# Optimization experiments

Measured on AMD Instinct MI355X. Metric: run time of the kernel, lower is better.

## Reference

```python
import jax, jax.numpy as jnp
import numpy as np


def setup_inputs() -> dict:
    key = jax.random.key(0)
    k1, k2 = jax.random.split(key)
    B, N, M, D = 4, 8192, 8192, 3
    pred_points = jax.random.normal(k1, (B, N, D), dtype=jnp.float32)
    gt_points = jax.random.normal(k2, (B, M, D), dtype=jnp.float32)
    return {"pred_points": pred_points, "gt_points": gt_points}


def reference(pred_points, gt_points):
    p2 = jnp.sum(pred_points * pred_points, axis=-1)  # [B, N]
    g2 = jnp.sum(gt_points * gt_points, axis=-1)      # [B, M]
    cross = jnp.einsum("bnd,bmd->bnm", pred_points, gt_points)  # [B, N, M]
    d2 = p2[:, :, None] + g2[:, None, :] - 2.0 * cross
    dist = jnp.sqrt(jnp.maximum(d2, 0.0))             # [B, N, M]
    min_pred_to_gt = jnp.min(dist, axis=-1)           # [B, N]
    min_gt_to_pred = jnp.min(dist, axis=-2)           # [B, M]
    return min_pred_to_gt.mean() + min_gt_to_pred.mean()
```

## Files before the change

### kernel.cpp

```cpp
#include <hip/hip_runtime.h>


#define B_ 4
#define N_ 8192
#define QPT 4
#define THREADS 256

__global__ __launch_bounds__(THREADS) void chamfer_min2(
    const float* __restrict__ pred, const float* __restrict__ gt,
    float* __restrict__ partial) {
  extern __shared__ float4 sh[];
  const int S = gridDim.y;
  const int TPB = N_ / S;
  const int dirb = blockIdx.z;
  const int dir = dirb >> 2;
  const int b = dirb & 3;

  const float* qsrc = (dir == 0 ? pred : gt) + (size_t)b * N_ * 3;
  const float* tsrc = (dir == 0 ? gt : pred) + (size_t)b * N_ * 3;

  const float* tb = tsrc + (size_t)blockIdx.y * TPB * 3;
  for (int g = 0; g < TPB; g += THREADS * 4) {
    const int p0 = g + threadIdx.x * 4;
    if (p0 < TPB) {
      const float4 f0 = *(const float4*)(tb + 3 * p0);
      const float4 f1 = *(const float4*)(tb + 3 * p0 + 4);
      const float4 f2 = *(const float4*)(tb + 3 * p0 + 8);
      sh[p0 + 0] = make_float4(f0.x, f0.y, f0.z,
                               fmaf(f0.x, f0.x, fmaf(f0.y, f0.y, f0.z * f0.z)));
      sh[p0 + 1] = make_float4(f0.w, f1.x, f1.y,
                               fmaf(f0.w, f0.w, fmaf(f1.x, f1.x, f1.y * f1.y)));
      sh[p0 + 2] = make_float4(f1.z, f1.w, f2.x,
                               fmaf(f1.z, f1.z, fmaf(f1.w, f1.w, f2.x * f2.x)));
      sh[p0 + 3] = make_float4(f2.y, f2.z, f2.w,
                               fmaf(f2.y, f2.y, fmaf(f2.z, f2.z, f2.w * f2.w)));
    }
  }
  __syncthreads();

  const int qbase = blockIdx.x * (THREADS * QPT) + threadIdx.x;
  float nx[QPT], ny[QPT], nz[QPT], q2[QPT];
#pragma unroll
  for (int k = 0; k < QPT; ++k) {
    const int qi = qbase + k * THREADS;
    const float x = qsrc[3 * qi], y = qsrc[3 * qi + 1], z = qsrc[3 * qi + 2];
    nx[k] = -2.0f * x; ny[k] = -2.0f * y; nz[k] = -2.0f * z;
    q2[k] = fmaf(x, x, fmaf(y, y, z * z));
  }

  float acc0[QPT], acc1[QPT];
#pragma unroll
  for (int k = 0; k < QPT; ++k) { acc0[k] = 3.4e38f; acc1[k] = 3.4e38f; }

  for (int j = 0; j < TPB; j += 4) {
    const float4 t0 = sh[j + 0];
    const float4 t1 = sh[j + 1];
    const float4 t2 = sh[j + 2];
    const float4 t3 = sh[j + 3];
#pragma unroll
    for (int k = 0; k < QPT; ++k) {
      const float s0 = fmaf(nx[k], t0.x, fmaf(ny[k], t0.y, fmaf(nz[k], t0.z, t0.w)));
      const float s1 = fmaf(nx[k], t1.x, fmaf(ny[k], t1.y, fmaf(nz[k], t1.z, t1.w)));
      const float s2 = fmaf(nx[k], t2.x, fmaf(ny[k], t2.y, fmaf(nz[k], t2.z, t2.w)));
      const float s3 = fmaf(nx[k], t3.x, fmaf(ny[k], t3.y, fmaf(nz[k], t3.z, t3.w)));
      acc0[k] = fminf(fminf(acc0[k], s0), s1);
      acc1[k] = fminf(fminf(acc1[k], s2), s3);
    }
  }

  float* dst = partial + ((size_t)dirb * S + blockIdx.y) * N_;
#pragma unroll
  for (int k = 0; k < QPT; ++k) {
    const int qi = qbase + k * THREADS;
    dst[qi] = fmaxf(q2[k] + fminf(acc0[k], acc1[k]), 0.0f);
  }
}

#define FBLOCKS 64
__global__ __launch_bounds__(256) void chamfer_finalize(
    const float* __restrict__ partial, float* __restrict__ out, int S) {
  float sum = 0.0f;
  const int total = 8 * N_;
  for (int f = blockIdx.x * 256 + threadIdx.x; f < total; f += FBLOCKS * 256) {
    const int dirb = f >> 13;
    const int qi = f & (N_ - 1);
    const float* p = partial + (size_t)dirb * S * N_ + qi;
    float v = p[0];
    for (int s = 1; s < S; ++s) v = fminf(v, p[(size_t)s * N_]);
    sum += sqrtf(v);
  }
#pragma unroll
  for (int off = 32; off > 0; off >>= 1) sum += __shfl_down(sum, off, 64);
  __shared__ float ws[4];
  const int lane = threadIdx.x & 63;
  const int wid = threadIdx.x >> 6;
  if (lane == 0) ws[wid] = sum;
  __syncthreads();
  if (threadIdx.x == 0) {
    atomicAdd(out, ((ws[0] + ws[1]) + (ws[2] + ws[3])) * (1.0f / 32768.0f));
  }
}

extern "C" void kernel_launch(void* const* d_in, const int* in_sizes, int n_in,
                              void* d_out, int out_size, void* d_ws, size_t ws_size,
                              hipStream_t stream) {
  const float* pred = (const float*)d_in[0];
  const float* gt   = (const float*)d_in[1];
  float* out = (float*)d_out;
  float* partial = (float*)d_ws;

  int S = 4;
  if (ws_size >= (size_t)8 * 16 * N_ * sizeof(float)) S = 16;
  else if (ws_size >= (size_t)8 * 8 * N_ * sizeof(float)) S = 8;

  hipMemsetAsync(out, 0, sizeof(float), stream);

  dim3 grid(N_ / (THREADS * QPT), S, 2 * B_);
  const size_t shbytes = (size_t)(N_ / S) * sizeof(float4);
  chamfer_min2<<<grid, THREADS, shbytes, stream>>>(pred, gt, partial);
  chamfer_finalize<<<FBLOCKS, 256, 0, stream>>>(partial, out, S);
}
```

Before: 109.2 us.

## Raise queries per thread, fix 32-way target split, use v_min3, drop memset

Doubles queries per thread to 8 and fixes the target split at 32 slices of 256 points each, with static shared memory, so each thread loads one target point. The inner loop uses the v_min3_f32 instruction to fold two distances into the running minimum per instruction. The finalize kernel reads float4 vectors across the 32 partial slices and writes the output through a last-block-done counter, which replaces the hipMemsetAsync call. The changes cut launch overhead and ALU instructions, but the grid becomes 4x32x8 blocks and the workspace must now hold 32 partial slices whatever ws_size is.

```diff
diff --git a/kernel.cpp b/kernel.cpp
--- a/kernel.cpp
+++ b/kernel.cpp
@@ -3,101 +3,111 @@
 
 #define B_ 4
 #define N_ 8192
-#define QPT 4
+#define QPT 8
 #define THREADS 256
+#define S_ 32
+#define TT (N_ / S_)
+
+__device__ __forceinline__ float min3f(float a, float b, float c) {
+  float d;
+  asm("v_min3_f32 %0, %1, %2, %3" : "=v"(d) : "v"(a), "v"(b), "v"(c));
+  return d;
+}
 
 __global__ __launch_bounds__(THREADS) void chamfer_min2(
     const float* __restrict__ pred, const float* __restrict__ gt,
-    float* __restrict__ partial) {
-  extern __shared__ float4 sh[];
-  const int S = gridDim.y;
-  const int TPB = N_ / S;
+    float* __restrict__ partial, float* __restrict__ accws) {
+  __shared__ float4 sh[TT];
+
+  const int tid = threadIdx.x;
   const int dirb = blockIdx.z;
   const int dir = dirb >> 2;
   const int b = dirb & 3;
 
+  if (blockIdx.x == 0 && blockIdx.y == 0 && blockIdx.z == 0 && tid < 2)
+    ((unsigned*)accws)[tid] = 0u;
+
   const float* qsrc = (dir == 0 ? pred : gt) + (size_t)b * N_ * 3;
   const float* tsrc = (dir == 0 ? gt : pred) + (size_t)b * N_ * 3;
 
-  const float* tb = tsrc + (size_t)blockIdx.y * TPB * 3;
-  for (int g = 0; g < TPB; g += THREADS * 4) {
-    const int p0 = g + threadIdx.x * 4;
-    if (p0 < TPB) {
-      const float4 f0 = *(const float4*)(tb + 3 * p0);
-      const float4 f1 = *(const float4*)(tb + 3 * p0 + 4);
-      const float4 f2 = *(const float4*)(tb + 3 * p0 + 8);
-      sh[p0 + 0] = make_float4(f0.x, f0.y, f0.z,
-                               fmaf(f0.x, f0.x, fmaf(f0.y, f0.y, f0.z * f0.z)));
-      sh[p0 + 1] = make_float4(f0.w, f1.x, f1.y,
-                               fmaf(f0.w, f0.w, fmaf(f1.x, f1.x, f1.y * f1.y)));
-      sh[p0 + 2] = make_float4(f1.z, f1.w, f2.x,
-                               fmaf(f1.z, f1.z, fmaf(f1.w, f1.w, f2.x * f2.x)));
-      sh[p0 + 3] = make_float4(f2.y, f2.z, f2.w,
-                               fmaf(f2.y, f2.y, fmaf(f2.z, f2.z, f2.w * f2.w)));
-    }
+  {
+    const float* tb = tsrc + (size_t)blockIdx.y * TT * 3;
+    const float x = tb[3 * tid], y = tb[3 * tid + 1], z = tb[3 * tid + 2];
+    sh[tid] = make_float4(x, y, z, fmaf(x, x, fmaf(y, y, z * z)));
   }
   __syncthreads();
 
-  const int qbase = blockIdx.x * (THREADS * QPT) + threadIdx.x;
-  float nx[QPT], ny[QPT], nz[QPT], q2[QPT];
+  const int qbase = blockIdx.x * (THREADS * QPT) + tid;
+  float nx[QPT], ny[QPT], nz[QPT], q2[QPT], acc[QPT];
 #pragma unroll
   for (int k = 0; k < QPT; ++k) {
     const int qi = qbase + k * THREADS;
     const float x = qsrc[3 * qi], y = qsrc[3 * qi + 1], z = qsrc[3 * qi + 2];
     nx[k] = -2.0f * x; ny[k] = -2.0f * y; nz[k] = -2.0f * z;
     q2[k] = fmaf(x, x, fmaf(y, y, z * z));
+    acc[k] = 3.4e38f;
   }
 
-  float acc0[QPT], acc1[QPT];
+  for (int j0 = 0; j0 < TT; j0 += 16) {
 #pragma unroll
-  for (int k = 0; k < QPT; ++k) { acc0[k] = 3.4e38f; acc1[k] = 3.4e38f; }
-
-  for (int j = 0; j < TPB; j += 4) {
-    const float4 t0 = sh[j + 0];
-    const float4 t1 = sh[j + 1];
-    const float4 t2 = sh[j + 2];
-    const float4 t3 = sh[j + 3];
+    for (int jj = 0; jj < 16; jj += 2) {
+      const float4 t0 = sh[j0 + jj];
+      const float4 t1 = sh[j0 + jj + 1];
 #pragma unroll
-    for (int k = 0; k < QPT; ++k) {
-      const float s0 = fmaf(nx[k], t0.x, fmaf(ny[k], t0.y, fmaf(nz[k], t0.z, t0.w)));
-      const float s1 = fmaf(nx[k], t1.x, fmaf(ny[k], t1.y, fmaf(nz[k], t1.z, t1.w)));
-      const float s2 = fmaf(nx[k], t2.x, fmaf(ny[k], t2.y, fmaf(nz[k], t2.z, t2.w)));
-      const float s3 = fmaf(nx[k], t3.x, fmaf(ny[k], t3.y, fmaf(nz[k], t3.z, t3.w)));
-      acc0[k] = fminf(fminf(acc0[k], s0), s1);
-      acc1[k] = fminf(fminf(acc1[k], s2), s3);
+      for (int k = 0; k < QPT; ++k) {
+        const float s0 = fmaf(nx[k], t0.x, fmaf(ny[k], t0.y, fmaf(nz[k], t0.z, t0.w)));
+        const float s1 = fmaf(nx[k], t1.x, fmaf(ny[k], t1.y, fmaf(nz[k], t1.z, t1.w)));
+        acc[k] = min3f(acc[k], s0, s1);
+      }
     }
   }
 
-  float* dst = partial + ((size_t)dirb * S + blockIdx.y) * N_;
+  float* dst = partial + ((size_t)dirb * S_ + blockIdx.y) * N_;
 #pragma unroll
   for (int k = 0; k < QPT; ++k) {
     const int qi = qbase + k * THREADS;
-    dst[qi] = fmaxf(q2[k] + fminf(acc0[k], acc1[k]), 0.0f);
+    dst[qi] = fmaxf(q2[k] + acc[k], 0.0f);
   }
 }
 
-#define FBLOCKS 64
-__global__ __launch_bounds__(256) void chamfer_finalize(
-    const float* __restrict__ partial, float* __restrict__ out, int S) {
-  float sum = 0.0f;
-  const int total = 8 * N_;
-  for (int f = blockIdx.x * 256 + threadIdx.x; f < total; f += FBLOCKS * 256) {
-    const int dirb = f >> 13;
-    const int qi = f & (N_ - 1);
-    const float* p = partial + (size_t)dirb * S * N_ + qi;
-    float v = p[0];
-    for (int s = 1; s < S; ++s) v = fminf(v, p[(size_t)s * N_]);
-    sum += sqrtf(v);
+__global__ __launch_bounds__(256) void chamfer_fin(
+    const float* __restrict__ partial, float* __restrict__ accws,
+    float* __restrict__ out) {
+  const int t = blockIdx.x * 256 + threadIdx.x;
+  const int base = t * 4;
+  const int dirb = base >> 13;
+  const int qi = base & (N_ - 1);
+
+  const float4* p = (const float4*)(partial + (size_t)dirb * S_ * N_ + qi);
+  const int stride4 = N_ / 4;
+  float4 m = p[0];
+#pragma unroll
+  for (int s = 1; s < S_; s += 2) {
+    const float4 a = p[(size_t)s * stride4];
+    const float4 c = p[(size_t)(s + 1 < S_ ? s + 1 : s) * stride4];
+    m.x = min3f(m.x, a.x, c.x);
+    m.y = min3f(m.y, a.y, c.y);
+    m.z = min3f(m.z, a.z, c.z);
+    m.w = min3f(m.w, a.w, c.w);
   }
+  float sum = sqrtf(m.x) + sqrtf(m.y) + sqrtf(m.z) + sqrtf(m.w);
+
 #pragma unroll
   for (int off = 32; off > 0; off >>= 1) sum += __shfl_down(sum, off, 64);
-  __shared__ float ws[4];
-  const int lane = threadIdx.x & 63;
-  const int wid = threadIdx.x >> 6;
-  if (lane == 0) ws[wid] = sum;
+  __shared__ float ws4[4];
+  const int lane = threadIdx.x & 63, wid = threadIdx.x >> 6;
+  if (lane == 0) ws4[wid] = sum;
   __syncthreads();
   if (threadIdx.x == 0) {
-    atomicAdd(out, ((ws[0] + ws[1]) + (ws[2] + ws[3])) * (1.0f / 32768.0f));
+    const float bs = (ws4[0] + ws4[1]) + (ws4[2] + ws4[3]);
+    atomicAdd(&accws[0], bs);
+    __threadfence();
+    const unsigned old = atomicAdd(((unsigned*)accws) + 1, 1u);
+    if (old == gridDim.x - 1) {
+      __threadfence();
+      const float tot = atomicAdd(&accws[0], 0.0f);
+      out[0] = tot * (1.0f / 32768.0f);
+    }
   }
 }
 
@@ -107,16 +117,11 @@
   const float* pred = (const float*)d_in[0];
   const float* gt   = (const float*)d_in[1];
   float* out = (float*)d_out;
-  float* partial = (float*)d_ws;
 
-  int S = 4;
-  if (ws_size >= (size_t)8 * 16 * N_ * sizeof(float)) S = 16;
-  else if (ws_size >= (size_t)8 * 8 * N_ * sizeof(float)) S = 8;
+  float* accws = (float*)d_ws;
+  float* partial = (float*)((char*)d_ws + 64);
 
-  hipMemsetAsync(out, 0, sizeof(float), stream);
-
-  dim3 grid(N_ / (THREADS * QPT), S, 2 * B_);
-  const size_t shbytes = (size_t)(N_ / S) * sizeof(float4);
-  chamfer_min2<<<grid, THREADS, shbytes, stream>>>(pred, gt, partial);
-  chamfer_finalize<<<FBLOCKS, 256, 0, stream>>>(partial, out, S);
+  chamfer_min2<<<dim3(N_ / (THREADS * QPT), S_, 2 * B_), THREADS, 0, stream>>>(
+      pred, gt, partial, accws);
+  chamfer_fin<<<64, 256, 0, stream>>>(partial, accws, out);
 }
```

Measured after the change: 100.7 us. 7.8% less time.
